# Performance work log

Measured on AMD Instinct MI355X. Metric: run time of the kernel, lower is better.

## Reference

```python
import jax, jax.numpy as jnp
import numpy as np

N = 100000      # nodes
E = 1600000     # edges (avg degree 16)
D = 64          # in_dim == hidden_dim
L = 4           # layer_gin
G = 128         # graphs in batch
BN_EPS = 1e-5


def setup_inputs() -> dict:
    key = jax.random.key(0)
    ks = jax.random.split(key, 9)
    x = jax.random.normal(ks[0], (N, D), dtype=jnp.float32)
    edge_index = jax.random.randint(ks[1], (2, E), 0, N, dtype=jnp.int32)
    batch = jnp.sort(jax.random.randint(ks[2], (N,), 0, G, dtype=jnp.int32))
    s = 0.05
    W1 = jax.random.normal(ks[3], (L, D, D), dtype=jnp.float32) * s
    b1 = jax.random.normal(ks[4], (L, D), dtype=jnp.float32) * s
    gamma = jnp.ones((L, D), dtype=jnp.float32)
    beta = jnp.zeros((L, D), dtype=jnp.float32)
    W2 = jax.random.normal(ks[5], (L, D, D), dtype=jnp.float32) * s
    b2 = jax.random.normal(ks[6], (L, D), dtype=jnp.float32) * s
    return dict(x=x, edge_index=edge_index, batch=batch,
                W1=W1, b1=b1, gamma=gamma, beta=beta, W2=W2, b2=b2)


def reference(x, edge_index, batch, W1, b1, gamma, beta, W2, b2):
    n = x.shape[0]
    src, dst = edge_index[0], edge_index[1]  # flow source_to_target
    # in-degree for mean aggregation (clamped to avoid div-by-zero)
    deg = jax.ops.segment_sum(jnp.ones(src.shape, x.dtype), dst, num_segments=n)
    inv_deg = 1.0 / jnp.maximum(deg, 1.0)
    # graph sizes for global mean pool
    gcnt = jax.ops.segment_sum(jnp.ones((n,), x.dtype), batch, num_segments=G)
    inv_gcnt = 1.0 / jnp.maximum(gcnt, 1.0)

    h = x
    node_pool = jnp.zeros((n, W2.shape[-1]), x.dtype)
    g_pool = jnp.zeros((G, W2.shape[-1]), x.dtype)
    for l in range(L):  # small fixed layer count
        # scatter-mean neighbor aggregation: [E,D] gather -> segment_sum
        agg = jax.ops.segment_sum(h[src], dst, num_segments=n) * inv_deg[:, None]
        z = (h + agg) @ W1[l] + b1[l]          # eps=0: (1+eps)*x + mean_j x_j
        mu = z.mean(axis=0)
        var = z.var(axis=0)                     # biased, as torch BatchNorm1d
        z = (z - mu) * jax.lax.rsqrt(var + BN_EPS) * gamma[l] + beta[l]
        h = jax.nn.relu(z) @ W2[l] + b2[l]
        node_pool = node_pool + h
        g_pool = g_pool + jax.ops.segment_sum(h, batch, num_segments=G) * inv_gcnt[:, None]
    return node_pool, g_pool
```

## Files before the change

kernel.cpp:

```cpp
#include <hip/hip_runtime.h>

#define N_NODES 100000
#define N_EDGES 1600000
#define DIM 64
#define NLAYER 4
#define NGRAPH 128
#define BN_EPS 1e-5f
#define NSHARD 16
#define AGG_CHUNK 16

typedef unsigned short ushort_t;
typedef unsigned int uint_t;
typedef __attribute__((ext_vector_type(8))) short short8;
typedef __attribute__((ext_vector_type(4))) float f32x4;

__device__ __forceinline__ ushort_t f2bf(float f) {
    uint_t u = __float_as_uint(f);
    uint_t r = (u + 0x7FFFu + ((u >> 16) & 1u)) >> 16;
    return (ushort_t)r;
}
__device__ __forceinline__ void bf8_to_f32(const uint4 v, float f[8]) {
    f[0] = __uint_as_float(v.x << 16);
    f[1] = __uint_as_float(v.x & 0xFFFF0000u);
    f[2] = __uint_as_float(v.y << 16);
    f[3] = __uint_as_float(v.y & 0xFFFF0000u);
    f[4] = __uint_as_float(v.z << 16);
    f[5] = __uint_as_float(v.z & 0xFFFF0000u);
    f[6] = __uint_as_float(v.w << 16);
    f[7] = __uint_as_float(v.w & 0xFFFF0000u);
}


__global__ void k_hist(const int* __restrict__ ei, int* __restrict__ cntS,
                       int* __restrict__ rank) {
    int e = blockIdx.x * blockDim.x + threadIdx.x;
    if (e < N_EDGES) {
        int d = ei[N_EDGES + e];
        int s = blockIdx.x & (NSHARD - 1);
        rank[e] = atomicAdd(&cntS[s * N_NODES + d], 1);
    }
}

__global__ void k_sumsh(int* __restrict__ cntS, int* __restrict__ cnt) {
    int i = blockIdx.x * blockDim.x + threadIdx.x;
    if (i < N_NODES) {
        int run = 0;
#pragma unroll
        for (int s = 0; s < NSHARD; s++) {
            int c = cntS[s * N_NODES + i];
            cntS[s * N_NODES + i] = run;
            run += c;
        }
        cnt[i] = run;
    }
}

__global__ void k_scan1(const int* __restrict__ cnt, int* __restrict__ exc,
                        int* __restrict__ bsums) {
    __shared__ int s[256];
    int i = blockIdx.x * 256 + threadIdx.x;
    int v = (i < N_NODES) ? cnt[i] : 0;
    s[threadIdx.x] = v;
    __syncthreads();
    for (int off = 1; off < 256; off <<= 1) {
        int t = (threadIdx.x >= off) ? s[threadIdx.x - off] : 0;
        __syncthreads();
        s[threadIdx.x] += t;
        __syncthreads();
    }
    if (i < N_NODES) exc[i] = s[threadIdx.x] - v;
    if (threadIdx.x == 255) bsums[blockIdx.x] = s[255];
}

__global__ void k_scan2(const int* __restrict__ bsums, int* __restrict__ boffs, int nb) {
    __shared__ int s[512];
    int v = ((int)threadIdx.x < nb) ? bsums[threadIdx.x] : 0;
    s[threadIdx.x] = v;
    __syncthreads();
    for (int off = 1; off < 512; off <<= 1) {
        int t = (threadIdx.x >= off) ? s[threadIdx.x - off] : 0;
        __syncthreads();
        s[threadIdx.x] += t;
        __syncthreads();
    }
    if ((int)threadIdx.x < nb) boffs[threadIdx.x] = s[threadIdx.x] - v;
}

__global__ void k_scan3(int* __restrict__ exc, const int* __restrict__ boffs) {
    int i = blockIdx.x * 256 + threadIdx.x;
    if (i < N_NODES) exc[i] += boffs[blockIdx.x];
}

__global__ void k_fill(const int* __restrict__ ei, const int* __restrict__ rowptr,
                       const int* __restrict__ cntS, const int* __restrict__ rank,
                       int* __restrict__ csr) {
    int e = blockIdx.x * blockDim.x + threadIdx.x;
    if (e < N_EDGES) {
        int d = ei[N_EDGES + e];
        int s = blockIdx.x & (NSHARD - 1);
        csr[rowptr[d] + cntS[s * N_NODES + d] + rank[e]] = ei[e];
    }
}

__global__ void k_prep(const int* __restrict__ cnt, const int* __restrict__ batch,
                       float* __restrict__ invdeg, float* __restrict__ invg) {
    int i = blockIdx.x * blockDim.x + threadIdx.x;
    if (i < N_NODES) invdeg[i] = 1.0f / (float)max(cnt[i], 1);
    if (i < NGRAPH) {
        int key = i, lo = 0, hi = N_NODES;
        while (lo < hi) { int m = (lo + hi) >> 1; if (batch[m] < key) lo = m + 1; else hi = m; }
        int a = lo;
        key = i + 1; lo = 0; hi = N_NODES;
        while (lo < hi) { int m = (lo + hi) >> 1; if (batch[m] < key) lo = m + 1; else hi = m; }
        invg[i] = 1.0f / (float)max(lo - a, 1);
    }
}

__global__ void k_xcast(const float* __restrict__ x, ushort_t* __restrict__ xh) {
    int i = blockIdx.x * blockDim.x + threadIdx.x;
    if (i < N_NODES * 16) {
        const float4 v = ((const float4*)x)[i];
        ushort4 u;
        u.x = f2bf(v.x); u.y = f2bf(v.y); u.z = f2bf(v.z); u.w = f2bf(v.w);
        ((ushort4*)xh)[i] = u;
    }
}

__device__ __forceinline__ void grp8b(const ushort_t* __restrict__ h,
                                      const int* __restrict__ cp,
                                      int e, int deg, int q, int r,
                                      float acc[8]) {
    const int last = deg - 1;
    const int e0 = e + q;
    int i0 = cp[min(e0, last)];
    float m0 = (e0 < deg) ? 1.f : 0.f;
    const uint4 v = *(const uint4*)(h + (size_t)i0 * 64 + r * 8);
    float f[8];
    bf8_to_f32(v, f);
#pragma unroll
    for (int j = 0; j < 8; j++) acc[j] = fmaf(f[j], m0, acc[j]);
}


__global__ __launch_bounds__(256, 4)
void k_passA(const ushort_t* __restrict__ h, const float* __restrict__ W1,
             const float* __restrict__ b1,
             const int* __restrict__ rowptr, const int* __restrict__ cnt,
             const int* __restrict__ csr, const float* __restrict__ invdeg,
             float* __restrict__ z, float* __restrict__ colsum,
             float* __restrict__ colsumsq) {
    __shared__ ushort_t wfrag[512 * 8];
    __shared__ uint_t smt[4][16 * 36];
    __shared__ float red[128];

    const int w = threadIdx.x >> 6;
    const int lane = threadIdx.x & 63;
    const int q = lane >> 3;
    const int r = lane & 7;
    const int wid = __builtin_amdgcn_readfirstlane((blockIdx.x << 2) | w);
    const bool active = wid < (N_NODES / AGG_CHUNK);
    const int n0 = (active ? wid : 0) * AGG_CHUNK;

    for (int s = threadIdx.x; s < 512; s += 256) {
        const int hh = s >> 8, c = (s >> 6) & 3, L = s & 63;
        const int kb = hh * 32 + ((L >> 4) * 8);
        const int out = c * 16 + (L & 15);
        uint_t* dst = (uint_t*)&wfrag[s * 8];
#pragma unroll
        for (int j2 = 0; j2 < 4; j2++) {
            const float lo = W1[(kb + 2 * j2) * 64 + out];
            const float hi = W1[(kb + 2 * j2 + 1) * 64 + out];
            dst[j2] = (uint_t)f2bf(lo) | ((uint_t)f2bf(hi) << 16);
        }
    }
    if (threadIdx.x < 128) red[threadIdx.x] = 0.f;
    __syncthreads();

    if (active) {
        for (int pp = 0; pp < AGG_CHUNK; pp += 2) {
            const int n = n0 + pp;
            const int sa = rowptr[n],     da = cnt[n];
            const int sb = rowptr[n + 1], db = cnt[n + 1];
            const float idga = invdeg[n], idgb = invdeg[n + 1];
            const int* __restrict__ ca = csr + sa;
            const int* __restrict__ cb = csr + sb;

            float aa[8] = {0,0,0,0,0,0,0,0};
            float ab[8] = {0,0,0,0,0,0,0,0};
            const int mm = min(da, db);
            int e = 0;
            for (; e < mm; e += 8) {
                grp8b(h, ca, e, da, q, r, aa);
                grp8b(h, cb, e, db, q, r, ab);
            }
            for (; e < da; e += 8) grp8b(h, ca, e, da, q, r, aa);
            for (; e < db; e += 8) grp8b(h, cb, e, db, q, r, ab);

#pragma unroll
            for (int j = 0; j < 8; j++) {
                aa[j] += __shfl_xor(aa[j], 8, 64);
                aa[j] += __shfl_xor(aa[j], 16, 64);
                aa[j] += __shfl_xor(aa[j], 32, 64);
                ab[j] += __shfl_xor(ab[j], 8, 64);
                ab[j] += __shfl_xor(ab[j], 16, 64);
                ab[j] += __shfl_xor(ab[j], 32, 64);
            }

            const uint4 sva = *(const uint4*)(h + (size_t)n * 64 + r * 8);
            const uint4 svb = *(const uint4*)(h + (size_t)(n + 1) * 64 + r * 8);
            float sa8[8], sb8[8];
            bf8_to_f32(sva, sa8);
            bf8_to_f32(svb, sb8);
            float ta[8], tb[8];
#pragma unroll
            for (int j = 0; j < 8; j++) {
                ta[j] = fmaf(aa[j], idga, sa8[j]);
                tb[j] = fmaf(ab[j], idgb, sb8[j]);
            }

            if (q < 2) {
                const int row = pp + q;
                uint_t* dst = &smt[w][row * 36 + r * 4];
#pragma unroll
                for (int j2 = 0; j2 < 4; j2++) {
                    const float lo = q ? tb[2 * j2]     : ta[2 * j2];
                    const float hi = q ? tb[2 * j2 + 1] : ta[2 * j2 + 1];
                    dst[j2] = (uint_t)f2bf(lo) | ((uint_t)f2bf(hi) << 16);
                }
            }
        }
    }
    __syncthreads();

    const int m = lane & 15;
    const int quad = lane >> 4;
    const short8 a0 = *(const short8*)&smt[w][m * 36 + quad * 4];
    const short8 a1 = *(const short8*)&smt[w][m * 36 + 16 + quad * 4];

    float lsum[4], lsq[4];
#pragma unroll
    for (int c = 0; c < 4; c++) {
        const short8 b0 = *(const short8*)&wfrag[(size_t)(c * 64 + lane) * 8];
        const short8 b1f = *(const short8*)&wfrag[(size_t)((4 + c) * 64 + lane) * 8];
        f32x4 D = {0.f, 0.f, 0.f, 0.f};
        D = __builtin_amdgcn_mfma_f32_16x16x32_bf16(a0, b0, D, 0, 0, 0);
        D = __builtin_amdgcn_mfma_f32_16x16x32_bf16(a1, b1f, D, 0, 0, 0);
        const float bv = b1[c * 16 + m];
        float s = 0.f, sq = 0.f;
#pragma unroll
        for (int reg = 0; reg < 4; reg++) {
            const float zv = D[reg] + bv;
            if (active) {
                const int node = n0 + quad * 4 + reg;
                z[(size_t)node * 64 + c * 16 + m] = zv;
            }
            s += zv;
            sq += zv * zv;
        }
        lsum[c] = s;
        lsq[c] = sq;
    }

    if (active) {
#pragma unroll
        for (int c = 0; c < 4; c++) {
            float s = lsum[c], sq = lsq[c];
            s += __shfl_xor(s, 16, 64);
            s += __shfl_xor(s, 32, 64);
            sq += __shfl_xor(sq, 16, 64);
            sq += __shfl_xor(sq, 32, 64);
            if (quad == 0) {
                atomicAdd(&red[c * 16 + m], s);
                atomicAdd(&red[64 + c * 16 + m], sq);
            }
        }
    }
    __syncthreads();
    if (threadIdx.x < 64) {
        atomicAdd(&colsum[threadIdx.x], red[threadIdx.x]);
        atomicAdd(&colsumsq[threadIdx.x], red[64 + threadIdx.x]);
    }
}


__global__ void k_bnprep(float* __restrict__ colsum, float* __restrict__ colsumsq,
                         const float* __restrict__ gamma, const float* __restrict__ beta,
                         float* __restrict__ scale, float* __restrict__ shift) {
    int j = threadIdx.x;
    float invn = 1.0f / (float)N_NODES;
    float mu = colsum[j] * invn;
    float var = colsumsq[j] * invn - mu * mu;
    float rsg = rsqrtf(var + BN_EPS);
    float sc = gamma[j] * rsg;
    scale[j] = sc;
    shift[j] = beta[j] - mu * sc;
    colsum[j] = 0.f;
    colsumsq[j] = 0.f;
}


#define CHUNK_M 28

__global__ __launch_bounds__(256, 4)
void k_passB(const float* __restrict__ z, const float* __restrict__ W2,
             const float* __restrict__ b2, const float* __restrict__ scale,
             const float* __restrict__ shift, const int* __restrict__ batch,
             ushort_t* __restrict__ hout, float* __restrict__ node_pool,
             float* __restrict__ gacc, int first) {
    const int lane = threadIdx.x & 63;
    int wid_raw = (blockIdx.x << 2) | (threadIdx.x >> 6);
    const int wid = __builtin_amdgcn_readfirstlane(wid_raw);
    const int n0 = wid * CHUNK_M;
    const int n1 = min(N_NODES, n0 + CHUNK_M);

    float w[64];
#pragma unroll
    for (int k = 0; k < 64; k++) w[k] = W2[k * 64 + lane];
#pragma unroll
    for (int k = 0; k < 64; k++) asm("" : "+v"(w[k]));
    const float bj = b2[lane], sc = scale[lane], sh = shift[lane];

    int curg = -1;
    float ga = 0.f;
    for (int n = n0; n + 4 <= n1; n += 4) {
        float ra = fmaxf(fmaf(z[(size_t)n * 64 + lane], sc, sh), 0.f);
        float rb = fmaxf(fmaf(z[(size_t)(n + 1) * 64 + lane], sc, sh), 0.f);
        float rc = fmaxf(fmaf(z[(size_t)(n + 2) * 64 + lane], sc, sh), 0.f);
        float rd = fmaxf(fmaf(z[(size_t)(n + 3) * 64 + lane], sc, sh), 0.f);
        float ha = bj, hb = bj, hc = bj, hd = bj;
#pragma unroll
        for (int k = 0; k < 64; k++) {
            float ka = __int_as_float(__builtin_amdgcn_readlane(__float_as_int(ra), k));
            float kb = __int_as_float(__builtin_amdgcn_readlane(__float_as_int(rb), k));
            float kc = __int_as_float(__builtin_amdgcn_readlane(__float_as_int(rc), k));
            float kd = __int_as_float(__builtin_amdgcn_readlane(__float_as_int(rd), k));
            ha = fmaf(ka, w[k], ha);
            hb = fmaf(kb, w[k], hb);
            hc = fmaf(kc, w[k], hc);
            hd = fmaf(kd, w[k], hd);
        }
        hout[(size_t)n * 64 + lane] = f2bf(ha);
        hout[(size_t)(n + 1) * 64 + lane] = f2bf(hb);
        hout[(size_t)(n + 2) * 64 + lane] = f2bf(hc);
        hout[(size_t)(n + 3) * 64 + lane] = f2bf(hd);
        if (first) {
            node_pool[(size_t)n * 64 + lane] = ha;
            node_pool[(size_t)(n + 1) * 64 + lane] = hb;
            node_pool[(size_t)(n + 2) * 64 + lane] = hc;
            node_pool[(size_t)(n + 3) * 64 + lane] = hd;
        } else {
            node_pool[(size_t)n * 64 + lane] += ha;
            node_pool[(size_t)(n + 1) * 64 + lane] += hb;
            node_pool[(size_t)(n + 2) * 64 + lane] += hc;
            node_pool[(size_t)(n + 3) * 64 + lane] += hd;
        }
        float hv[4] = {ha, hb, hc, hd};
#pragma unroll
        for (int j = 0; j < 4; j++) {
            int g = batch[n + j];
            if (g != curg) {
                if (curg >= 0) atomicAdd(&gacc[curg * 64 + lane], ga);
                ga = 0.f;
                curg = g;
            }
            ga += hv[j];
        }
    }
    if (curg >= 0) atomicAdd(&gacc[curg * 64 + lane], ga);
}

__global__ void k_gfinal(const float* __restrict__ gacc, const float* __restrict__ invg,
                         float* __restrict__ gout) {
    int i = blockIdx.x * blockDim.x + threadIdx.x;
    if (i < NGRAPH * 64) gout[i] = gacc[i] * invg[i >> 6];
}


extern "C" void kernel_launch(void* const* d_in, const int* in_sizes, int n_in,
                              void* d_out, int out_size, void* d_ws, size_t ws_size,
                              hipStream_t stream) {
    (void)in_sizes; (void)n_in; (void)out_size; (void)ws_size;
    const float* x     = (const float*)d_in[0];
    const int*   ei    = (const int*)d_in[1];
    const int*   batch = (const int*)d_in[2];
    const float* W1    = (const float*)d_in[3];
    const float* b1    = (const float*)d_in[4];
    const float* gamma = (const float*)d_in[5];
    const float* beta  = (const float*)d_in[6];
    const float* W2    = (const float*)d_in[7];
    const float* b2    = (const float*)d_in[8];
    float* out = (float*)d_out;

    size_t o = 0;
    size_t o_cntS    = o; o += (size_t)NSHARD * N_NODES;
    size_t o_colsum  = o; o += 64;
    size_t o_colsq   = o; o += 64;
    size_t o_gacc    = o; o += (size_t)NGRAPH * 64;
    size_t zero_elems = o;
    size_t o_cnt     = o; o += N_NODES;
    size_t o_rowptr  = o; o += N_NODES;
    size_t o_bsums   = o; o += 512;
    size_t o_boffs   = o; o += 512;
    size_t o_invdeg  = o; o += N_NODES;
    size_t o_invg    = o; o += NGRAPH;
    size_t o_scale   = o; o += 64;
    size_t o_shift   = o; o += 64;
    size_t o_rank    = o; o += N_EDGES;
    size_t o_csr     = o; o += N_EDGES;
    size_t o_bufA    = o; o += (size_t)N_NODES * 64;
    size_t o_bufB    = o; o += (size_t)N_NODES * 16;
    size_t o_xh      = o; o += (size_t)N_NODES * 16;

    int*   wsi = (int*)d_ws;
    float* wsf = (float*)d_ws;
    int*      cntS   = wsi + o_cntS;
    float*    colsum = wsf + o_colsum;
    float*    colsq  = wsf + o_colsq;
    float*    gacc   = wsf + o_gacc;
    int*      cnt    = wsi + o_cnt;
    int*      rowptr = wsi + o_rowptr;
    int*      bsums  = wsi + o_bsums;
    int*      boffs  = wsi + o_boffs;
    float*    invdeg = wsf + o_invdeg;
    float*    invg   = wsf + o_invg;
    float*    scale  = wsf + o_scale;
    float*    shift  = wsf + o_shift;
    int*      rank   = wsi + o_rank;
    int*      csr    = wsi + o_csr;
    float*    bufA   = wsf + o_bufA;
    ushort_t* bufB   = (ushort_t*)(wsi + o_bufB);
    ushort_t* xh     = (ushort_t*)(wsi + o_xh);

    hipMemsetAsync(d_ws, 0, zero_elems * 4, stream);

    const int eb = (N_EDGES + 255) / 256;
    const int nb = (N_NODES + 255) / 256;

    k_hist<<<eb, 256, 0, stream>>>(ei, cntS, rank);
    k_xcast<<<(N_NODES * 16 + 255) / 256, 256, 0, stream>>>(x, xh);
    k_sumsh<<<nb, 256, 0, stream>>>(cntS, cnt);
    k_scan1<<<nb, 256, 0, stream>>>(cnt, rowptr, bsums);
    k_scan2<<<1, 512, 0, stream>>>(bsums, boffs, nb);
    k_scan3<<<nb, 256, 0, stream>>>(rowptr, boffs);
    k_prep<<<nb, 256, 0, stream>>>(cnt, batch, invdeg, invg);
    k_fill<<<eb, 256, 0, stream>>>(ei, rowptr, cntS, rank, csr);

    const int gridA = (N_NODES / AGG_CHUNK + 3) / 4;
    const int gridM = (N_NODES + CHUNK_M * 4 - 1) / (CHUNK_M * 4);
    for (int l = 0; l < NLAYER; l++) {
        const ushort_t* h_in = (l == 0) ? xh : bufB;
        k_passA<<<gridA, 256, 0, stream>>>(h_in, W1 + l * 4096, b1 + l * 64,
                                           rowptr, cnt, csr, invdeg,
                                           bufA, colsum, colsq);
        k_bnprep<<<1, 64, 0, stream>>>(colsum, colsq, gamma + l * 64, beta + l * 64,
                                       scale, shift);
        k_passB<<<gridM, 256, 0, stream>>>(bufA, W2 + l * 4096, b2 + l * 64,
                                           scale, shift, batch,
                                           bufB, out, gacc, (l == 0) ? 1 : 0);
    }
    k_gfinal<<<32, 256, 0, stream>>>(gacc, invg, out + (size_t)N_NODES * 64);
}
```

Before: 644.7 us.

## Use MFMA for second linear layer, fold BN prep, defer pooling to one pass

The second per-layer linear transform moves from a readlane-based scalar FMA loop to bf16 MFMA tiles of 16 nodes, with BN scale and shift computed inside the kernel so the separate bnprep launch goes away. Node-pool and graph-pool accumulation leave the per-layer kernel. Instead, all four layer outputs are kept as bf16 buffers and a single pool kernel sums them at the end, which removes three read-modify-write passes over node_pool. Intermediate z stores and loads become nontemporal. In exchange, node_pool is now summed from bf16-rounded activations, and the second matmul input is quantised to bf16, both of which lose precision.

```diff
diff --git a/kernel.cpp b/kernel.cpp
--- a/kernel.cpp
+++ b/kernel.cpp
@@ -18,6 +18,9 @@
     uint_t u = __float_as_uint(f);
     uint_t r = (u + 0x7FFFu + ((u >> 16) & 1u)) >> 16;
     return (ushort_t)r;
+}
+__device__ __forceinline__ float bf2f(ushort_t u) {
+    return __uint_as_float((uint_t)u << 16);
 }
 __device__ __forceinline__ void bf8_to_f32(const uint4 v, float f[8]) {
     f[0] = __uint_as_float(v.x << 16);
@@ -252,7 +255,7 @@
             const float zv = D[reg] + bv;
             if (active) {
                 const int node = n0 + quad * 4 + reg;
-                z[(size_t)node * 64 + c * 16 + m] = zv;
+                __builtin_nontemporal_store(zv, &z[(size_t)node * 64 + c * 16 + m]);
             }
             s += zv;
             sq += zv * zv;
@@ -283,88 +286,124 @@
 }
 
 
-__global__ void k_bnprep(float* __restrict__ colsum, float* __restrict__ colsumsq,
-                         const float* __restrict__ gamma, const float* __restrict__ beta,
-                         float* __restrict__ scale, float* __restrict__ shift) {
-    int j = threadIdx.x;
-    float invn = 1.0f / (float)N_NODES;
-    float mu = colsum[j] * invn;
-    float var = colsumsq[j] * invn - mu * mu;
-    float rsg = rsqrtf(var + BN_EPS);
-    float sc = gamma[j] * rsg;
-    scale[j] = sc;
-    shift[j] = beta[j] - mu * sc;
-    colsum[j] = 0.f;
-    colsumsq[j] = 0.f;
-}
-
-
-#define CHUNK_M 28
-
 __global__ __launch_bounds__(256, 4)
 void k_passB(const float* __restrict__ z, const float* __restrict__ W2,
-             const float* __restrict__ b2, const float* __restrict__ scale,
-             const float* __restrict__ shift, const int* __restrict__ batch,
-             ushort_t* __restrict__ hout, float* __restrict__ node_pool,
-             float* __restrict__ gacc, int first) {
+             const float* __restrict__ b2, const float* __restrict__ colsum,
+             const float* __restrict__ colsumsq, const float* __restrict__ gamma,
+             const float* __restrict__ beta, ushort_t* __restrict__ hout) {
+    __shared__ ushort_t wfrag[512 * 8];
+    __shared__ float sscale[64], sshift[64];
+    __shared__ float ltile[4][16 * 68];
+
+    const int w = threadIdx.x >> 6;
     const int lane = threadIdx.x & 63;
-    int wid_raw = (blockIdx.x << 2) | (threadIdx.x >> 6);
-    const int wid = __builtin_amdgcn_readfirstlane(wid_raw);
-    const int n0 = wid * CHUNK_M;
-    const int n1 = min(N_NODES, n0 + CHUNK_M);
-
-    float w[64];
-#pragma unroll
-    for (int k = 0; k < 64; k++) w[k] = W2[k * 64 + lane];
-#pragma unroll
-    for (int k = 0; k < 64; k++) asm("" : "+v"(w[k]));
-    const float bj = b2[lane], sc = scale[lane], sh = shift[lane];
-
+    const int wid = __builtin_amdgcn_readfirstlane((blockIdx.x << 2) | w);
+    const bool active = wid < (N_NODES / 16);
+    const int n0 = (active ? wid : 0) * 16;
+
+    for (int s = threadIdx.x; s < 512; s += 256) {
+        const int hh = s >> 8, c = (s >> 6) & 3, L = s & 63;
+        const int kb = hh * 32 + ((L >> 4) * 8);
+        const int out = c * 16 + (L & 15);
+        uint_t* dst = (uint_t*)&wfrag[s * 8];
+#pragma unroll
+        for (int j2 = 0; j2 < 4; j2++) {
+            const float lo = W2[(kb + 2 * j2) * 64 + out];
+            const float hi = W2[(kb + 2 * j2 + 1) * 64 + out];
+            dst[j2] = (uint_t)f2bf(lo) | ((uint_t)f2bf(hi) << 16);
+        }
+    }
+    if (threadIdx.x < 64) {
+        const float invn = 1.0f / (float)N_NODES;
+        const float mu = colsum[threadIdx.x] * invn;
+        const float var = colsumsq[threadIdx.x] * invn - mu * mu;
+        const float sc = gamma[threadIdx.x] * rsqrtf(var + BN_EPS);
+        sscale[threadIdx.x] = sc;
+        sshift[threadIdx.x] = beta[threadIdx.x] - mu * sc;
+    }
+    __syncthreads();
+
+    const int m = lane & 15;
+    const int quad = lane >> 4;
+
+    const float* zp = z + (size_t)(n0 + m) * 64;
+    const f32x4 za = __builtin_nontemporal_load((const f32x4*)(zp + quad * 8));
+    const f32x4 zb = __builtin_nontemporal_load((const f32x4*)(zp + quad * 8 + 4));
+    const f32x4 zc = __builtin_nontemporal_load((const f32x4*)(zp + 32 + quad * 8));
+    const f32x4 zd = __builtin_nontemporal_load((const f32x4*)(zp + 32 + quad * 8 + 4));
+    const f32x4 c0 = *(const f32x4*)&sscale[quad * 8];
+    const f32x4 c1 = *(const f32x4*)&sscale[quad * 8 + 4];
+    const f32x4 c2 = *(const f32x4*)&sscale[32 + quad * 8];
+    const f32x4 c3 = *(const f32x4*)&sscale[32 + quad * 8 + 4];
+    const f32x4 h0 = *(const f32x4*)&sshift[quad * 8];
+    const f32x4 h1v = *(const f32x4*)&sshift[quad * 8 + 4];
+    const f32x4 h2v = *(const f32x4*)&sshift[32 + quad * 8];
+    const f32x4 h3v = *(const f32x4*)&sshift[32 + quad * 8 + 4];
+
+    float r0[8], r1[8];
+#pragma unroll
+    for (int j = 0; j < 4; j++) {
+        r0[j]     = fmaxf(fmaf(za[j], c0[j], h0[j]), 0.f);
+        r0[4 + j] = fmaxf(fmaf(zb[j], c1[j], h1v[j]), 0.f);
+        r1[j]     = fmaxf(fmaf(zc[j], c2[j], h2v[j]), 0.f);
+        r1[4 + j] = fmaxf(fmaf(zd[j], c3[j], h3v[j]), 0.f);
+    }
+    union { uint_t u[4]; short8 v; } pa0, pa1;
+#pragma unroll
+    for (int j2 = 0; j2 < 4; j2++) {
+        pa0.u[j2] = (uint_t)f2bf(r0[2 * j2]) | ((uint_t)f2bf(r0[2 * j2 + 1]) << 16);
+        pa1.u[j2] = (uint_t)f2bf(r1[2 * j2]) | ((uint_t)f2bf(r1[2 * j2 + 1]) << 16);
+    }
+    const short8 a0 = pa0.v;
+    const short8 a1 = pa1.v;
+
+#pragma unroll
+    for (int c = 0; c < 4; c++) {
+        const short8 b0 = *(const short8*)&wfrag[(size_t)(c * 64 + lane) * 8];
+        const short8 b1f = *(const short8*)&wfrag[(size_t)((4 + c) * 64 + lane) * 8];
+        f32x4 D = {0.f, 0.f, 0.f, 0.f};
+        D = __builtin_amdgcn_mfma_f32_16x16x32_bf16(a0, b0, D, 0, 0, 0);
+        D = __builtin_amdgcn_mfma_f32_16x16x32_bf16(a1, b1f, D, 0, 0, 0);
+        const float bv = b2[c * 16 + m];
+#pragma unroll
+        for (int reg = 0; reg < 4; reg++)
+            ltile[w][(quad * 4 + reg) * 68 + c * 16 + m] = D[reg] + bv;
+    }
+
+    if (active) {
+#pragma unroll
+        for (int n = 0; n < 16; n++) {
+            const float hv = ltile[w][n * 68 + lane];
+            hout[(size_t)(n0 + n) * 64 + lane] = f2bf(hv);
+        }
+    }
+}
+
+
+#define POOL_CHUNK 64
+
+__global__ void k_pool(const ushort_t* __restrict__ h1, const ushort_t* __restrict__ h2,
+                       const ushort_t* __restrict__ h3, const ushort_t* __restrict__ h4,
+                       const int* __restrict__ batch, float* __restrict__ node_pool,
+                       float* __restrict__ gacc) {
+    const int lane = threadIdx.x & 63;
+    const int wid = (blockIdx.x << 2) | (threadIdx.x >> 6);
+    const int n0 = wid * POOL_CHUNK;
+    if (n0 >= N_NODES) return;
+    const int n1 = min(N_NODES, n0 + POOL_CHUNK);
     int curg = -1;
     float ga = 0.f;
-    for (int n = n0; n + 4 <= n1; n += 4) {
-        float ra = fmaxf(fmaf(z[(size_t)n * 64 + lane], sc, sh), 0.f);
-        float rb = fmaxf(fmaf(z[(size_t)(n + 1) * 64 + lane], sc, sh), 0.f);
-        float rc = fmaxf(fmaf(z[(size_t)(n + 2) * 64 + lane], sc, sh), 0.f);
-        float rd = fmaxf(fmaf(z[(size_t)(n + 3) * 64 + lane], sc, sh), 0.f);
-        float ha = bj, hb = bj, hc = bj, hd = bj;
-#pragma unroll
-        for (int k = 0; k < 64; k++) {
-            float ka = __int_as_float(__builtin_amdgcn_readlane(__float_as_int(ra), k));
-            float kb = __int_as_float(__builtin_amdgcn_readlane(__float_as_int(rb), k));
-            float kc = __int_as_float(__builtin_amdgcn_readlane(__float_as_int(rc), k));
-            float kd = __int_as_float(__builtin_amdgcn_readlane(__float_as_int(rd), k));
-            ha = fmaf(ka, w[k], ha);
-            hb = fmaf(kb, w[k], hb);
-            hc = fmaf(kc, w[k], hc);
-            hd = fmaf(kd, w[k], hd);
-        }
-        hout[(size_t)n * 64 + lane] = f2bf(ha);
-        hout[(size_t)(n + 1) * 64 + lane] = f2bf(hb);
-        hout[(size_t)(n + 2) * 64 + lane] = f2bf(hc);
-        hout[(size_t)(n + 3) * 64 + lane] = f2bf(hd);
-        if (first) {
-            node_pool[(size_t)n * 64 + lane] = ha;
-            node_pool[(size_t)(n + 1) * 64 + lane] = hb;
-            node_pool[(size_t)(n + 2) * 64 + lane] = hc;
-            node_pool[(size_t)(n + 3) * 64 + lane] = hd;
-        } else {
-            node_pool[(size_t)n * 64 + lane] += ha;
-            node_pool[(size_t)(n + 1) * 64 + lane] += hb;
-            node_pool[(size_t)(n + 2) * 64 + lane] += hc;
-            node_pool[(size_t)(n + 3) * 64 + lane] += hd;
-        }
-        float hv[4] = {ha, hb, hc, hd};
-#pragma unroll
-        for (int j = 0; j < 4; j++) {
-            int g = batch[n + j];
-            if (g != curg) {
-                if (curg >= 0) atomicAdd(&gacc[curg * 64 + lane], ga);
-                ga = 0.f;
-                curg = g;
-            }
-            ga += hv[j];
-        }
+    for (int n = n0; n < n1; n++) {
+        const size_t off = (size_t)n * 64 + lane;
+        const float v = bf2f(h1[off]) + bf2f(h2[off]) + bf2f(h3[off]) + bf2f(h4[off]);
+        __builtin_nontemporal_store(v, &node_pool[off]);
+        const int g = batch[n];
+        if (g != curg) {
+            if (curg >= 0) atomicAdd(&gacc[curg * 64 + lane], ga);
+            ga = 0.f;
+            curg = g;
+        }
+        ga += v;
     }
     if (curg >= 0) atomicAdd(&gacc[curg * 64 + lane], ga);
 }
@@ -393,8 +432,8 @@
 
     size_t o = 0;
     size_t o_cntS    = o; o += (size_t)NSHARD * N_NODES;
-    size_t o_colsum  = o; o += 64;
-    size_t o_colsq   = o; o += 64;
+    size_t o_colsum  = o; o += (size_t)NLAYER * 64;
+    size_t o_colsq   = o; o += (size_t)NLAYER * 64;
     size_t o_gacc    = o; o += (size_t)NGRAPH * 64;
     size_t zero_elems = o;
     size_t o_cnt     = o; o += N_NODES;
@@ -403,13 +442,13 @@
     size_t o_boffs   = o; o += 512;
     size_t o_invdeg  = o; o += N_NODES;
     size_t o_invg    = o; o += NGRAPH;
-    size_t o_scale   = o; o += 64;
-    size_t o_shift   = o; o += 64;
     size_t o_rank    = o; o += N_EDGES;
     size_t o_csr     = o; o += N_EDGES;
     size_t o_bufA    = o; o += (size_t)N_NODES * 64;
-    size_t o_bufB    = o; o += (size_t)N_NODES * 16;
-    size_t o_xh      = o; o += (size_t)N_NODES * 16;
+    size_t o_h1      = o; o += (size_t)N_NODES * 32;
+    size_t o_h2      = o; o += (size_t)N_NODES * 32;
+    size_t o_h3      = o; o += (size_t)N_NODES * 32;
+    size_t o_xh      = o; o += (size_t)N_NODES * 32;
 
     int*   wsi = (int*)d_ws;
     float* wsf = (float*)d_ws;
@@ -423,12 +462,12 @@
     int*      boffs  = wsi + o_boffs;
     float*    invdeg = wsf + o_invdeg;
     float*    invg   = wsf + o_invg;
-    float*    scale  = wsf + o_scale;
-    float*    shift  = wsf + o_shift;
     int*      rank   = wsi + o_rank;
     int*      csr    = wsi + o_csr;
     float*    bufA   = wsf + o_bufA;
-    ushort_t* bufB   = (ushort_t*)(wsi + o_bufB);
+    ushort_t* hb0    = (ushort_t*)(wsi + o_h1);
+    ushort_t* hb1    = (ushort_t*)(wsi + o_h2);
+    ushort_t* hb2    = (ushort_t*)(wsi + o_h3);
     ushort_t* xh     = (ushort_t*)(wsi + o_xh);
 
     hipMemsetAsync(d_ws, 0, zero_elems * 4, stream);
@@ -445,18 +484,19 @@
     k_prep<<<nb, 256, 0, stream>>>(cnt, batch, invdeg, invg);
     k_fill<<<eb, 256, 0, stream>>>(ei, rowptr, cntS, rank, csr);
 
+    const ushort_t* hin[NLAYER]  = {xh,  hb0, hb1, hb2};
+    ushort_t*       hoz[NLAYER]  = {hb0, hb1, hb2, xh};
+
     const int gridA = (N_NODES / AGG_CHUNK + 3) / 4;
-    const int gridM = (N_NODES + CHUNK_M * 4 - 1) / (CHUNK_M * 4);
     for (int l = 0; l < NLAYER; l++) {
-        const ushort_t* h_in = (l == 0) ? xh : bufB;
-        k_passA<<<gridA, 256, 0, stream>>>(h_in, W1 + l * 4096, b1 + l * 64,
+        k_passA<<<gridA, 256, 0, stream>>>(hin[l], W1 + l * 4096, b1 + l * 64,
                                            rowptr, cnt, csr, invdeg,
-                                           bufA, colsum, colsq);
-        k_bnprep<<<1, 64, 0, stream>>>(colsum, colsq, gamma + l * 64, beta + l * 64,
-                                       scale, shift);
-        k_passB<<<gridM, 256, 0, stream>>>(bufA, W2 + l * 4096, b2 + l * 64,
-                                           scale, shift, batch,
-                                           bufB, out, gacc, (l == 0) ? 1 : 0);
-    }
+                                           bufA, colsum + l * 64, colsq + l * 64);
+        k_passB<<<gridA, 256, 0, stream>>>(bufA, W2 + l * 4096, b2 + l * 64,
+                                           colsum + l * 64, colsq + l * 64,
+                                           gamma + l * 64, beta + l * 64, hoz[l]);
+    }
+    const int gridP = (N_NODES + POOL_CHUNK * 4 - 1) / (POOL_CHUNK * 4);
+    k_pool<<<gridP, 256, 0, stream>>>(hb0, hb1, hb2, xh, batch, out, gacc);
     k_gfinal<<<32, 256, 0, stream>>>(gacc, invg, out + (size_t)N_NODES * 64);
 }
```

Measured after the change: 571.7 us. 1.13x faster.
